# Kernel optimization log

Measured on AMD Instinct MI355X. Metric: run time of the kernel, lower is better.

The kernel has to match this reference:

```python
import jax, jax.numpy as jnp
import numpy as np

BN_EPS = 1e-5
NUM_SUBSET = 3


def _conv1x1(x, W, b):
    # x: [B,C,T,J], W: [O,C], b: [O] -> [B,O,T,J]
    return jnp.einsum('bctj,oc->botj', x, W) + b[:, None, None]


def _bn_eval(y, gamma, beta, mean, var):
    inv = gamma / jnp.sqrt(var + BN_EPS)
    return y * inv[:, None, None] + (beta - mean * inv)[:, None, None]


def setup_inputs() -> dict:
    key = jax.random.key(0)
    ks = jax.random.split(key, 8)
    B, Cin, T, J = 64, 64, 300, 25
    Cout, inter = 128, 32
    s = 0.05
    return {
        'x': jax.random.normal(ks[0], (B, Cin, T, J), jnp.float32),
        'PA': jax.random.normal(ks[1], (NUM_SUBSET, J, J), jnp.float32) * s,
        'Wa': jax.random.normal(ks[2], (NUM_SUBSET, inter, Cin), jnp.float32) * s,
        'ba': jnp.zeros((NUM_SUBSET, inter), jnp.float32),
        'Wb': jax.random.normal(ks[3], (NUM_SUBSET, inter, Cin), jnp.float32) * s,
        'bb': jnp.zeros((NUM_SUBSET, inter), jnp.float32),
        'Wd': jax.random.normal(ks[4], (NUM_SUBSET, Cout, Cin), jnp.float32) * s,
        'bd': jnp.zeros((NUM_SUBSET, Cout), jnp.float32),
        'Wdown': jax.random.normal(ks[5], (Cout, Cin), jnp.float32) * s,
        'bdown': jnp.zeros((Cout,), jnp.float32),
        'bn_gamma': jnp.ones((Cout,), jnp.float32),
        'bn_beta': jnp.zeros((Cout,), jnp.float32),
        'bn_mean': jnp.zeros((Cout,), jnp.float32),
        'bn_var': jnp.ones((Cout,), jnp.float32),
        'down_gamma': jnp.ones((Cout,), jnp.float32),
        'down_beta': jnp.zeros((Cout,), jnp.float32),
        'down_mean': jnp.zeros((Cout,), jnp.float32),
        'down_var': jnp.ones((Cout,), jnp.float32),
    }


def reference(x, PA, Wa, ba, Wb, bb, Wd, bd, Wdown, bdown,
              bn_gamma, bn_beta, bn_mean, bn_var,
              down_gamma, down_beta, down_mean, down_var):
    B, C, T, J = x.shape
    A = PA + jnp.eye(J, dtype=x.dtype)  # [S,J,J]
    x_flat = x.reshape(B, C * T, J)
    y = None
    for i in range(NUM_SUBSET):
        # theta/phi embeddings via 1x1 convs -> [B,inter,T,J]
        A1 = _conv1x1(x, Wa[i], ba[i])
        A2 = _conv1x1(x, Wb[i], bb[i])
        A1 = A1.transpose(0, 3, 1, 2).reshape(B, J, -1)  # [B,J,inter*T]
        A2 = A2.reshape(B, -1, J)                          # [B,inter*T,J]
        scores = jnp.matmul(A1, A2) / A1.shape[-1]         # [B,J,J]
        Aadapt = jax.nn.softmax(scores, axis=-2) + A[i]    # softmax over dim -2
        z = jnp.matmul(x_flat, Aadapt).reshape(B, C, T, J)
        z = _conv1x1(z, Wd[i], bd[i])                      # [B,Cout,T,J]
        y = z if y is None else y + z
    y = _bn_eval(y, bn_gamma, bn_beta, bn_mean, bn_var)
    res = _bn_eval(_conv1x1(x, Wdown, bdown), down_gamma, down_beta, down_mean, down_var)
    return jax.nn.relu(y + res)
```

## Files before the change

kernel.cpp:

```cpp
#include <hip/hip_runtime.h>
#include <math.h>

#define T_DIM 300
#define J_DIM 25
#define CIN 64
#define COUT 128
#define B_DIM 64

typedef __attribute__((ext_vector_type(8))) short bf16x8;
typedef __attribute__((ext_vector_type(4))) float f32x4;

__device__ __forceinline__ unsigned short f2bf(float f) {
    union { float f; unsigned u; } v; v.f = f;
    unsigned r = v.u + 0x7FFF + ((v.u >> 16) & 1);
    return (unsigned short)(r >> 16);
}

__device__ __forceinline__ unsigned pkbf(float lo, float hi) {
    return (unsigned)f2bf(lo) | ((unsigned)f2bf(hi) << 16);
}

#define SC_NSEG 10
#define SC_NCH  3

__global__ __launch_bounds__(256, 2) void scores_kernel(
    const float* __restrict__ x,
    const float* __restrict__ Wa, const float* __restrict__ ba,
    const float* __restrict__ Wb, const float* __restrict__ bb,
    float* __restrict__ part)
{
    __shared__ uint4 xsf[8][256];
    __shared__ unsigned short aT1[32][328];
    __shared__ unsigned short aT2[32][328];

    const int tid  = threadIdx.x;
    const int seg  = blockIdx.x;
    const int b    = blockIdx.y;
    const int lane = tid & 63;
    const int w    = tid >> 6;
    const int g4   = lane >> 4;
    const int c16  = lane & 15;
    const int jt1  = w >> 1, jt2 = w & 1;

    const float* xb = x + (size_t)b * (CIN * T_DIM * J_DIM);

    f32x4 gacc[3];
    #pragma unroll
    for (int i = 0; i < 3; ++i) gacc[i] = (f32x4){0.f, 0.f, 0.f, 0.f};

    for (int ch = 0; ch < SC_NCH; ++ch) {
        const int pb = seg * 750 + ch * 250;

        #pragma unroll
        for (int cg = 0; cg < 8; ++cg) {
            int p = pb + tid; if (p > 7499) p = 7499;
            const float* xc = xb + (size_t)(cg * 8) * 7500 + p;
            unsigned d[4];
            #pragma unroll
            for (int m = 0; m < 4; ++m)
                d[m] = (unsigned)f2bf(xc[(2 * m) * 7500]) |
                       ((unsigned)f2bf(xc[(2 * m + 1) * 7500]) << 16);
            xsf[cg][tid] = make_uint4(d[0], d[1], d[2], d[3]);
        }
        __syncthreads();

        #pragma unroll
        for (int i = 0; i < 3; ++i) {
            #pragma unroll
            for (int pass = 0; pass < 2; ++pass) {
                const float* W  = pass ? Wb : Wa;
                const float* bs = pass ? bb : ba;
                bf16x8 afr[2][2];
                #pragma unroll
                for (int m = 0; m < 2; ++m)
                    #pragma unroll
                    for (int s = 0; s < 2; ++s) {
                        const float* wp = W + i * 2048 + (m * 16 + c16) * 64 + s * 32 + g4 * 8;
                        float4 f0 = *(const float4*)(wp);
                        float4 f1 = *(const float4*)(wp + 4);
                        bf16x8 t;
                        t[0] = f2bf(f0.x); t[1] = f2bf(f0.y); t[2] = f2bf(f0.z); t[3] = f2bf(f0.w);
                        t[4] = f2bf(f1.x); t[5] = f2bf(f1.y); t[6] = f2bf(f1.z); t[7] = f2bf(f1.w);
                        afr[m][s] = t;
                    }
                f32x4 acc[2][4];
                #pragma unroll
                for (int m = 0; m < 2; ++m) {
                    float4 bv = *(const float4*)(bs + i * 32 + m * 16 + g4 * 4);
                    #pragma unroll
                    for (int n = 0; n < 4; ++n)
                        acc[m][n] = (f32x4){bv.x, bv.y, bv.z, bv.w};
                }
                #pragma unroll
                for (int n = 0; n < 4; ++n) {
                    const int ptile = w * 4 + n;
                    #pragma unroll
                    for (int s = 0; s < 2; ++s) {
                        bf16x8 bfr = *reinterpret_cast<const bf16x8*>(&xsf[s * 4 + g4][ptile * 16 + c16]);
                        #pragma unroll
                        for (int m = 0; m < 2; ++m)
                            acc[m][n] = __builtin_amdgcn_mfma_f32_16x16x32_bf16(
                                afr[m][s], bfr, acc[m][n], 0, 0, 0);
                    }
                }
                unsigned short (*aT)[328] = pass ? aT2 : aT1;
                #pragma unroll
                for (int n = 0; n < 4; ++n) {
                    const int pos = (w * 4 + n) * 16 + c16;
                    if (pos < 250) {
                        const int t = pos / 25, j = pos - t * 25;
                        #pragma unroll
                        for (int m = 0; m < 2; ++m) {
                            const int k = m * 16 + g4 * 4;
                            aT[j][(k + 0) * 10 + t] = f2bf(acc[m][n][0]);
                            aT[j][(k + 1) * 10 + t] = f2bf(acc[m][n][1]);
                            aT[j][(k + 2) * 10 + t] = f2bf(acc[m][n][2]);
                            aT[j][(k + 3) * 10 + t] = f2bf(acc[m][n][3]);
                        }
                    }
                }
            }
            __syncthreads();

            #pragma unroll
            for (int s = 0; s < 10; ++s) {
                bf16x8 af = *reinterpret_cast<const bf16x8*>(&aT1[jt1 * 16 + c16][s * 32 + g4 * 8]);
                bf16x8 bf = *reinterpret_cast<const bf16x8*>(&aT2[jt2 * 16 + c16][s * 32 + g4 * 8]);
                gacc[i] = __builtin_amdgcn_mfma_f32_16x16x32_bf16(af, bf, gacc[i], 0, 0, 0);
            }
            __syncthreads();
        }
    }

    #pragma unroll
    for (int i = 0; i < 3; ++i) {
        const int j2 = jt2 * 16 + c16;
        #pragma unroll
        for (int r = 0; r < 4; ++r) {
            const int j1 = jt1 * 16 + g4 * 4 + r;
            if (j1 < 25 && j2 < 25)
                part[((size_t)(b * 3 + i) * SC_NSEG + seg) * 625 + j1 * 25 + j2] = gacc[i][r];
        }
    }
}

__global__ void softmax_kernel(const float* __restrict__ part,
                               const float* __restrict__ PA,
                               uint4* __restrict__ Gbg)
{
    int bi = blockIdx.x;
    int b = bi / 3, i = bi - b * 3;
    int j2 = threadIdx.x;
    if (j2 >= 32) return;
    float gval[25];
    if (j2 < 25) {
        float v[25];
        float m = -1e30f;
        #pragma unroll
        for (int j1 = 0; j1 < 25; ++j1) {
            float s = 0.0f;
            for (int seg = 0; seg < SC_NSEG; ++seg)
                s += part[((size_t)bi * SC_NSEG + seg) * 625 + j1 * 25 + j2];
            v[j1] = s * (1.0f / 9600.0f);
            m = fmaxf(m, v[j1]);
        }
        float sum = 0.0f;
        #pragma unroll
        for (int j1 = 0; j1 < 25; ++j1) { v[j1] = expf(v[j1] - m); sum += v[j1]; }
        float r = 1.0f / sum;
        #pragma unroll
        for (int j1 = 0; j1 < 25; ++j1)
            gval[j1] = v[j1] * r + PA[(i * 25 + j1) * 25 + j2] + (j1 == j2 ? 1.0f : 0.0f);
    }
    #pragma unroll
    for (int kg = 0; kg < 4; ++kg) {
        unsigned d[4];
        #pragma unroll
        for (int mm = 0; mm < 4; ++mm) {
            int ja = kg * 8 + 2 * mm, jb2 = ja + 1;
            float va = (j2 < 25 && ja < 25) ? gval[ja] : 0.0f;
            float vb = (j2 < 25 && jb2 < 25) ? gval[jb2] : 0.0f;
            d[mm] = pkbf(va, vb);
        }
        Gbg[((size_t)bi * 4 + kg) * 33 + j2] = make_uint4(d[0], d[1], d[2], d[3]);
    }
}

__global__ void prep_kernel(
    const float* __restrict__ Wd, const float* __restrict__ bd,
    const float* __restrict__ Wdown, const float* __restrict__ bdown,
    const float* __restrict__ g1, const float* __restrict__ b1,
    const float* __restrict__ m1, const float* __restrict__ v1,
    const float* __restrict__ g2, const float* __restrict__ b2,
    const float* __restrict__ m2, const float* __restrict__ v2,
    unsigned short* __restrict__ Wpb, float* __restrict__ cst)
{
    const int tid = threadIdx.x;
    for (int idx = tid; idx < COUT * 256; idx += 256) {
        int o = idx >> 8, k = idx & 255;
        int region = k >> 6;
        float val;
        if (region == 1) {
            float inv = g2[o] * rsqrtf(v2[o] + 1e-5f);
            val = Wdown[o * 64 + (k & 63)] * inv;
        } else {
            int i = (region == 0) ? 0 : region - 1;
            float inv = g1[o] * rsqrtf(v1[o] + 1e-5f);
            val = Wd[(i * COUT + o) * 64 + (k & 63)] * inv;
        }
        Wpb[idx] = f2bf(val);
    }
    if (tid < COUT) {
        int o = tid;
        float inv1 = g1[o] * rsqrtf(v1[o] + 1e-5f);
        float inv2 = g2[o] * rsqrtf(v2[o] + 1e-5f);
        cst[o] = (bd[o] + bd[COUT + o] + bd[2 * COUT + o]) * inv1
               + (b1[o] - m1[o] * inv1)
               + bdown[o] * inv2
               + (b2[o] - m2[o] * inv2);
    }
}

#define M_NCH 75

__global__ __launch_bounds__(512, 4) void main_kernel(
    const float* __restrict__ x, const uint4* __restrict__ Gbg,
    const unsigned short* __restrict__ Wpb, const float* __restrict__ cst,
    float* __restrict__ out)
{
    __shared__ unsigned short xs_bf[64][136];
    __shared__ uint4 zxs[16][113];
    __shared__ uint4 gb[396];

    const int tid  = threadIdx.x;
    const int b    = blockIdx.y;
    const int t0   = blockIdx.x * 4;
    const int lane = tid & 63;
    const int w    = __builtin_amdgcn_readfirstlane(tid >> 6);
    const int g4   = lane >> 4;
    const int c16  = lane & 15;

    const float* xb = x + (size_t)b * (CIN * T_DIM * J_DIM) + t0 * 25;

    #pragma unroll
    for (int it = 0; it < 4; ++it) {
        const int u = tid + it * 512;
        const int quad = u & 7, t = (u >> 3) & 3, c = u >> 5;
        const int jp0 = quad * 4;
        float v[4];
        #pragma unroll
        for (int e = 0; e < 4; ++e) {
            const int jp = jp0 + e;
            v[e] = (jp < 25) ? xb[c * 7500 + t * 25 + jp] : 0.0f;
        }
        unsigned lo = pkbf(v[0], v[1]), hi = pkbf(v[2], v[3]);
        *reinterpret_cast<uint2*>(&xs_bf[c][t * 32 + jp0]) = make_uint2(lo, hi);
        const int kg = 8 + (c >> 3);
        const int sl = c & 7;
        #pragma unroll
        for (int e = 0; e < 4; ++e) {
            const int jp = jp0 + e;
            if (jp < 25)
                *((unsigned short*)&zxs[kg][t * 25 + jp] + sl) = f2bf(v[e]);
        }
    }
    if (tid < 396) gb[tid] = Gbg[(size_t)b * 396 + tid];

    f32x4 acc[7];
    #pragma unroll
    for (int n = 0; n < 7; ++n) acc[n] = (f32x4){0.f, 0.f, 0.f, 0.f};

    const int zt = w >> 1;
    const int mh = w & 1;

    __syncthreads();

    bf16x8 a_x[2];
    #pragma unroll
    for (int m = 0; m < 2; ++m)
        a_x[m] = *reinterpret_cast<const bf16x8*>(&xs_bf[(mh * 2 + m) * 16 + c16][zt * 32 + g4 * 8]);

    auto zpass = [&](int i, int kb) {
        #pragma unroll
        for (int n = 0; n < 2; ++n) {
            bf16x8 bfr = *reinterpret_cast<const bf16x8*>(&gb[(i * 4 + g4) * 33 + n * 16 + c16]);
            #pragma unroll
            for (int m = 0; m < 2; ++m) {
                f32x4 d = __builtin_amdgcn_mfma_f32_16x16x32_bf16(
                    a_x[m], bfr, (f32x4){0.f, 0.f, 0.f, 0.f}, 0, 0, 0);
                const int j = n * 16 + c16;
                if (j < 25) {
                    const int cb = (mh * 2 + m) * 16 + g4 * 4;
                    const int kg = kb + (cb >> 3);
                    const int hf = (cb >> 2) & 1;
                    unsigned lo = pkbf(d[0], d[1]), hi = pkbf(d[2], d[3]);
                    *reinterpret_cast<uint2*>(
                        reinterpret_cast<char*>(&zxs[kg][zt * 25 + j]) + hf * 8) = make_uint2(lo, hi);
                }
            }
        }
    };

    zpass(0, 0);
    __syncthreads();

    {
        const unsigned short* wrow = Wpb + (w * 16 + c16) * 256 + g4 * 8;
        #pragma unroll
        for (int kk = 0; kk < 4; ++kk) {
            bf16x8 afr = *reinterpret_cast<const bf16x8*>(wrow + kk * 32);
            #pragma unroll
            for (int n = 0; n < 7; ++n) {
                bf16x8 bfr = *reinterpret_cast<const bf16x8*>(&zxs[kk * 4 + g4][n * 16 + c16]);
                acc[n] = __builtin_amdgcn_mfma_f32_16x16x32_bf16(afr, bfr, acc[n], 0, 0, 0);
            }
        }
    }
    __syncthreads();

    zpass(1, 0);
    zpass(2, 8);
    __syncthreads();

    {
        const unsigned short* wrow = Wpb + (w * 16 + c16) * 256 + 128 + g4 * 8;
        #pragma unroll
        for (int kk = 0; kk < 4; ++kk) {
            bf16x8 afr = *reinterpret_cast<const bf16x8*>(wrow + kk * 32);
            #pragma unroll
            for (int n = 0; n < 7; ++n) {
                bf16x8 bfr = *reinterpret_cast<const bf16x8*>(&zxs[kk * 4 + g4][n * 16 + c16]);
                acc[n] = __builtin_amdgcn_mfma_f32_16x16x32_bf16(afr, bfr, acc[n], 0, 0, 0);
            }
        }
    }

    float* ob = out + (size_t)b * (COUT * T_DIM * J_DIM) + t0 * 25;
    #pragma unroll
    for (int r = 0; r < 4; ++r) {
        const int o = w * 16 + g4 * 4 + r;
        const float cv = cst[o];
        #pragma unroll
        for (int n = 0; n < 7; ++n) {
            const int pos = n * 16 + c16;
            if (pos < 100)
                ob[(size_t)o * 7500 + pos] = fmaxf(acc[n][r] + cv, 0.0f);
        }
    }
}

extern "C" void kernel_launch(void* const* d_in, const int* in_sizes, int n_in,
                              void* d_out, int out_size, void* d_ws, size_t ws_size,
                              hipStream_t stream)
{
    const float* x     = (const float*)d_in[0];
    const float* PA    = (const float*)d_in[1];
    const float* Wa    = (const float*)d_in[2];
    const float* ba    = (const float*)d_in[3];
    const float* Wb    = (const float*)d_in[4];
    const float* bb    = (const float*)d_in[5];
    const float* Wd    = (const float*)d_in[6];
    const float* bd    = (const float*)d_in[7];
    const float* Wdown = (const float*)d_in[8];
    const float* bdown = (const float*)d_in[9];
    const float* bn_g  = (const float*)d_in[10];
    const float* bn_b  = (const float*)d_in[11];
    const float* bn_m  = (const float*)d_in[12];
    const float* bn_v  = (const float*)d_in[13];
    const float* dn_g  = (const float*)d_in[14];
    const float* dn_b  = (const float*)d_in[15];
    const float* dn_m  = (const float*)d_in[16];
    const float* dn_v  = (const float*)d_in[17];

    float* ws   = (float*)d_ws;
    float* part = ws;
    uint4* Gbg  = (uint4*)(ws + 1200000);
    float* cst  = ws + 1301376;
    unsigned short* Wpb = (unsigned short*)(ws + 1301504);

    prep_kernel<<<1, 256, 0, stream>>>(Wd, bd, Wdown, bdown,
        bn_g, bn_b, bn_m, bn_v, dn_g, dn_b, dn_m, dn_v, Wpb, cst);
    scores_kernel<<<dim3(SC_NSEG, B_DIM), 256, 0, stream>>>(x, Wa, ba, Wb, bb, part);
    softmax_kernel<<<dim3(B_DIM * 3), 64, 0, stream>>>(part, PA, Gbg);
    main_kernel<<<dim3(M_NCH, B_DIM), 512, 0, stream>>>(x, Gbg, Wpb, cst, (float*)d_out);
}
```

Baseline: 276.4 us.

## Drop xs_bf and gb shared buffers, load MFMA operands directly from global

The main kernel no longer stages x as bf16 or the per-batch G matrix in shared memory. Each wave loads its MFMA A fragments straight from global x and reads G fragments directly from global. This cuts LDS use and one barrier, and the launch bound is raised to allow 8 blocks per CU. The price is redundant, uncoalesced global reads and more register pressure under the tighter launch bound. Separately, the score kernel's aT writes are changed to packed 8-byte stores with a new [t*32+k] layout, and the reader side must match that layout.

```diff
diff --git a/kernel.cpp b/kernel.cpp
--- a/kernel.cpp
+++ b/kernel.cpp
@@ -111,11 +111,10 @@
                         const int t = pos / 25, j = pos - t * 25;
                         #pragma unroll
                         for (int m = 0; m < 2; ++m) {
-                            const int k = m * 16 + g4 * 4;
-                            aT[j][(k + 0) * 10 + t] = f2bf(acc[m][n][0]);
-                            aT[j][(k + 1) * 10 + t] = f2bf(acc[m][n][1]);
-                            aT[j][(k + 2) * 10 + t] = f2bf(acc[m][n][2]);
-                            aT[j][(k + 3) * 10 + t] = f2bf(acc[m][n][3]);
+                            const int kbase = t * 32 + m * 16 + g4 * 4;
+                            uint2 pk = make_uint2(pkbf(acc[m][n][0], acc[m][n][1]),
+                                                  pkbf(acc[m][n][2], acc[m][n][3]));
+                            *reinterpret_cast<uint2*>(&aT[j][kbase]) = pk;
                         }
                     }
                 }
@@ -223,14 +222,12 @@
 
 #define M_NCH 75
 
-__global__ __launch_bounds__(512, 4) void main_kernel(
+__global__ __launch_bounds__(512, 8) void main_kernel(
     const float* __restrict__ x, const uint4* __restrict__ Gbg,
     const unsigned short* __restrict__ Wpb, const float* __restrict__ cst,
     float* __restrict__ out)
 {
-    __shared__ unsigned short xs_bf[64][136];
     __shared__ uint4 zxs[16][113];
-    __shared__ uint4 gb[396];
 
     const int tid  = threadIdx.x;
     const int b    = blockIdx.y;
@@ -247,24 +244,15 @@
         const int u = tid + it * 512;
         const int quad = u & 7, t = (u >> 3) & 3, c = u >> 5;
         const int jp0 = quad * 4;
-        float v[4];
-        #pragma unroll
-        for (int e = 0; e < 4; ++e) {
-            const int jp = jp0 + e;
-            v[e] = (jp < 25) ? xb[c * 7500 + t * 25 + jp] : 0.0f;
-        }
-        unsigned lo = pkbf(v[0], v[1]), hi = pkbf(v[2], v[3]);
-        *reinterpret_cast<uint2*>(&xs_bf[c][t * 32 + jp0]) = make_uint2(lo, hi);
         const int kg = 8 + (c >> 3);
         const int sl = c & 7;
         #pragma unroll
         for (int e = 0; e < 4; ++e) {
             const int jp = jp0 + e;
             if (jp < 25)
-                *((unsigned short*)&zxs[kg][t * 25 + jp] + sl) = f2bf(v[e]);
-        }
-    }
-    if (tid < 396) gb[tid] = Gbg[(size_t)b * 396 + tid];
+                *((unsigned short*)&zxs[kg][t * 25 + jp] + sl) = f2bf(xb[c * 7500 + t * 25 + jp]);
+        }
+    }
 
     f32x4 acc[7];
     #pragma unroll
@@ -273,17 +261,26 @@
     const int zt = w >> 1;
     const int mh = w & 1;
 
-    __syncthreads();
-
     bf16x8 a_x[2];
     #pragma unroll
-    for (int m = 0; m < 2; ++m)
-        a_x[m] = *reinterpret_cast<const bf16x8*>(&xs_bf[(mh * 2 + m) * 16 + c16][zt * 32 + g4 * 8]);
+    for (int m = 0; m < 2; ++m) {
+        const int cA = (mh * 2 + m) * 16 + c16;
+        const float* xrow = xb + cA * 7500 + zt * 25 + g4 * 8;
+        bf16x8 t;
+        #pragma unroll
+        for (int e = 0; e < 8; ++e) {
+            const int jp = g4 * 8 + e;
+            t[e] = (jp < 25) ? (short)f2bf(xrow[e]) : (short)0;
+        }
+        a_x[m] = t;
+    }
+
+    const uint4* gbb = Gbg + (size_t)b * 396;
 
     auto zpass = [&](int i, int kb) {
         #pragma unroll
         for (int n = 0; n < 2; ++n) {
-            bf16x8 bfr = *reinterpret_cast<const bf16x8*>(&gb[(i * 4 + g4) * 33 + n * 16 + c16]);
+            bf16x8 bfr = *reinterpret_cast<const bf16x8*>(&gbb[(i * 4 + g4) * 33 + n * 16 + c16]);
             #pragma unroll
             for (int m = 0; m < 2; ++m) {
                 f32x4 d = __builtin_amdgcn_mfma_f32_16x16x32_bf16(
```

After: 309.7 us. 1.12x slower.
